# Performance work log

Hardware: AMD Instinct MI355X
Metric: run time of the kernel (lower is better)

Reference implementation:

```python
import jax, jax.numpy as jnp
import numpy as np

B, S, D = 2, 2048, 1024
H, DK = 16, 64          # heads, d_k (= d_v)
DH = 4096               # FFN hidden
EPS = 1e-5


def _layer_norm(x, gamma, beta):
    mu = jnp.mean(x, axis=-1, keepdims=True)
    var = jnp.var(x, axis=-1, keepdims=True)
    return (x - mu) * jax.lax.rsqrt(var + EPS) * gamma + beta


def setup_inputs() -> dict:
    key = jax.random.key(0)
    ks = jax.random.split(key, 8)
    s = lambda fan_in: 1.0 / np.sqrt(fan_in)
    return {
        "x": jax.random.normal(ks[0], (B, S, D), dtype=jnp.float32),
        # NOTE: source module uses W_q for queries, keys AND values (bug kept faithfully),
        # so W_k / W_v are never used and are not materialized.
        "Wq": jax.random.normal(ks[1], (D, H * DK), dtype=jnp.float32) * s(D),
        "bq": jnp.zeros((H * DK,), dtype=jnp.float32),
        "Wo": jax.random.normal(ks[2], (H * DK, D), dtype=jnp.float32) * s(H * DK),
        "bo": jnp.zeros((D,), dtype=jnp.float32),
        "ln1_g": jnp.ones((D,), dtype=jnp.float32),
        "ln1_b": jnp.zeros((D,), dtype=jnp.float32),
        "W1": jax.random.normal(ks[3], (D, DH), dtype=jnp.float32) * s(D),
        "b1": jnp.zeros((DH,), dtype=jnp.float32),
        "W2": jax.random.normal(ks[4], (DH, D), dtype=jnp.float32) * s(DH),
        "b2": jnp.zeros((D,), dtype=jnp.float32),
        "ln2_g": jnp.ones((D,), dtype=jnp.float32),
        "ln2_b": jnp.zeros((D,), dtype=jnp.float32),
    }


def reference(x, Wq, bq, Wo, bo, ln1_g, ln1_b, W1, b1, W2, b2, ln2_g, ln2_b):
    residual = x
    # projections: q, k, v all use W_q (faithful to source)
    q = (x @ Wq + bq).reshape(B, S, H, DK)
    k = (x @ Wq + bq).reshape(B, S, H, DK)
    v = (x @ Wq + bq).reshape(B, S, H, DK)
    # scores scaled by sqrt(sequence_length), as in the source
    scale = 1.0 / jnp.sqrt(jnp.float32(S))
    scores = jnp.einsum("bqhd,bkhd->bhqk", q, k) * scale
    probs = jax.nn.softmax(scores, axis=-1)
    attn = jnp.einsum("bhqk,bkhd->bqhd", probs, v).reshape(B, S, H * DK)
    attn = attn @ Wo + bo
    # dropout is identity in eval mode
    x = _layer_norm(attn + residual, ln1_g, ln1_b)
    residual = x
    h = jax.nn.relu(x @ W1 + b1)
    x = h @ W2 + b2
    x = _layer_norm(x + residual, ln2_g, ln2_b)
    return x
```

## Files before the change

### kernel.cpp

```cpp
#include <hip/hip_runtime.h>
#include <stdint.h>


typedef unsigned short u16;
typedef __attribute__((ext_vector_type(8))) short v8s;
typedef __attribute__((ext_vector_type(4))) float v4f;
typedef __attribute__((ext_vector_type(16))) float v16f;
typedef __attribute__((ext_vector_type(2))) unsigned int v2u;

#define AS1 __attribute__((address_space(1)))
#define AS3 __attribute__((address_space(3)))

__device__ __forceinline__ void gl_lds16(const u16* g, u16* l) {
  __builtin_amdgcn_global_load_lds((const AS1 void*)g, (AS3 void*)l, 16, 0, 0);
}

__device__ __forceinline__ float bf2f(u16 u) {
  union { uint32_t i; float f; } v; v.i = ((uint32_t)u) << 16; return v.f;
}
__device__ __forceinline__ u16 f2bf(float f) {
  union { float f; uint32_t i; } v; v.f = f;
  uint32_t x = v.i;
  return (u16)((x + 0x7FFFu + ((x >> 16) & 1u)) >> 16);
}
__device__ __forceinline__ uint32_t fbits(float f) {
  union { float f; uint32_t u; } v; v.f = f; return v.u;
}

__global__ __launch_bounds__(256) void cvt_f2b(
    const float* __restrict__ src, u16* __restrict__ dst, int n4) {
  int i = (blockIdx.x * 256 + threadIdx.x);
  if (i < n4) {
    float4 v = *(const float4*)(src + (size_t)i * 4);
    ushort4 o;
    o.x = f2bf(v.x); o.y = f2bf(v.y); o.z = f2bf(v.z); o.w = f2bf(v.w);
    *(ushort4*)(dst + (size_t)i * 4) = o;
  }
}

__global__ __launch_bounds__(256) void transpose_f2b(
    const float* __restrict__ src, u16* __restrict__ dst,
    int R, int C, int ld_s, int ld_d) {
  __shared__ float tile[32][33];
  const int tx = threadIdx.x & 31, ty = threadIdx.x >> 5;
  const int c0 = blockIdx.x * 32, r0 = blockIdx.y * 32;
#pragma unroll
  for (int j = 0; j < 32; j += 8)
    tile[ty + j][tx] = src[(size_t)(r0 + ty + j) * ld_s + c0 + tx];
  __syncthreads();
#pragma unroll
  for (int j = 0; j < 32; j += 8)
    dst[(size_t)(c0 + ty + j) * ld_d + r0 + tx] = f2bf(tile[tx][ty + j]);
}

__global__ __launch_bounds__(256) void transpose_b2b(
    const u16* __restrict__ src, u16* __restrict__ dst,
    int R, int C, int ld_s, int ld_d) {
  __shared__ u16 tile[32][33];
  const int tx = threadIdx.x & 31, ty = threadIdx.x >> 5;
  const int c0 = blockIdx.x * 32, r0 = blockIdx.y * 32;
#pragma unroll
  for (int j = 0; j < 32; j += 8)
    tile[ty + j][tx] = src[(size_t)(r0 + ty + j) * ld_s + c0 + tx];
  __syncthreads();
#pragma unroll
  for (int j = 0; j < 32; j += 8)
    dst[(size_t)(c0 + ty + j) * ld_d + r0 + tx] = tile[tx][ty + j];
}

__global__ __launch_bounds__(512, 1) void gemm_8p(
    const u16* __restrict__ A, const u16* __restrict__ Bt,
    const float* __restrict__ bias, void* __restrict__ C0,
    u16* __restrict__ C1, u16* __restrict__ C2, u16* __restrict__ C3,
    int M, int N, int ldk, int klen, int relu, int c0_f32) {
  __shared__ u16 As[2][16384];
  __shared__ u16 Bs[2][16384];
  const int tid = threadIdx.x;
  const int w = tid >> 6, l = tid & 63;
  const int l16 = l & 15, kgrp = (l >> 4) & 3;
  const int wm = w >> 2, wn = w & 3;

  const int gx = gridDim.x, gyd = gridDim.y;
  const int nxy = gx * gyd;
  const int nwg = nxy * gridDim.z;
  int lin = blockIdx.x + gx * (blockIdx.y + gyd * blockIdx.z);
  if ((nwg & 7) == 0) lin = (lin & 7) * (nwg >> 3) + (lin >> 3);
  const int z = lin / nxy;
  const int rem = lin - z * nxy;
  const int by = rem / gx;
  const int bx = rem - by * gx;
  const int m0 = by * 256, n0 = bx * 256;
  const int NT = klen >> 6;

  const int rl = tid >> 3;
  const int sw = 8 * ((tid & 7) ^ (rl & 7));
  const u16* gA[4]; const u16* gB[4];
#pragma unroll
  for (int j = 0; j < 4; j++) {
    gA[j] = A + (size_t)(m0 + j * 64 + rl) * ldk + (size_t)z * klen + sw;
    gB[j] = Bt + (size_t)(n0 + j * 64 + rl) * ldk + (size_t)z * klen + sw;
  }
  const int sdst = w * 512;

  const int ch0 = 8 * ((kgrp) ^ (l16 & 7));
  const int ch1 = 8 * ((4 + kgrp) ^ (l16 & 7));
  const int abase = (wm * 128 + l16) * 64;
  const int bbase = (wn * 64 + l16) * 64;

  v4f acc[8][4];
#pragma unroll
  for (int i = 0; i < 8; i++)
#pragma unroll
    for (int j = 0; j < 4; j++)
#pragma unroll
      for (int r = 0; r < 4; r++) acc[i][j][r] = 0.f;

  v8s a[4][2], b[4][2];

#define FENCE() asm volatile("" ::: "memory")
#define VMC(n) asm volatile("s_waitcnt vmcnt(" #n ")" ::: "memory")
#define BARX() { __builtin_amdgcn_s_barrier(); \
                 __builtin_amdgcn_sched_barrier(0); FENCE(); }
#define STGA(q, j, kt) gl_lds16(gA[j] + (size_t)(kt) * 64, &As[q][(j) * 4096 + sdst])
#define STGB(q, j, kt) gl_lds16(gB[j] + (size_t)(kt) * 64, &Bs[q][(j) * 4096 + sdst])
#define LDA(p, mh) { \
  const u16* Ap = &As[p][abase + (mh) * 4096]; \
  _Pragma("unroll") for (int mi = 0; mi < 4; mi++) { \
    a[mi][0] = *(const v8s*)(Ap + mi * 1024 + ch0); \
    a[mi][1] = *(const v8s*)(Ap + mi * 1024 + ch1); } }
#define LDB(p, nh) { \
  const u16* Bp = &Bs[p][bbase + (nh) * 2048]; \
  _Pragma("unroll") for (int ni = 0; ni < 2; ni++) { \
    b[(nh) * 2 + ni][0] = *(const v8s*)(Bp + ni * 1024 + ch0); \
    b[(nh) * 2 + ni][1] = *(const v8s*)(Bp + ni * 1024 + ch1); } }
#define MFQ(mh, nh) { \
  __builtin_amdgcn_s_setprio(1); \
  _Pragma("unroll") for (int ks = 0; ks < 2; ks++) \
  _Pragma("unroll") for (int mi = 0; mi < 4; mi++) \
  _Pragma("unroll") for (int ni = 0; ni < 2; ni++) \
    acc[(mh) * 4 + mi][(nh) * 2 + ni] = __builtin_amdgcn_mfma_f32_16x16x32_bf16( \
        a[mi][ks], b[(nh) * 2 + ni][ks], acc[(mh) * 4 + mi][(nh) * 2 + ni], 0, 0, 0); \
  __builtin_amdgcn_s_setprio(0); }

  STGA(0, 0, 0); STGA(0, 2, 0);
  FENCE();
  STGB(0, 0, 0); STGB(0, 1, 0);
  FENCE();
  STGB(0, 2, 0); STGB(0, 3, 0);
  FENCE();
  STGA(0, 1, 0); STGA(0, 3, 0);

  int p = 0;
  for (int kt = 0; kt < NT - 1; ++kt, p ^= 1) {
    const int q = p ^ 1;
    const int kn = kt + 1;
    VMC(2); BARX();
    LDA(p, 0);
    LDB(p, 0);
    FENCE();
    STGA(q, 0, kn); STGA(q, 2, kn);
    MFQ(0, 0);
    LDB(p, 1);
    FENCE();
    STGB(q, 0, kn); STGB(q, 1, kn);
    STGB(q, 2, kn); STGB(q, 3, kn);
    MFQ(0, 1);
    VMC(6); BARX();
    LDA(p, 1);
    FENCE();
    STGA(q, 1, kn); STGA(q, 3, kn);
    MFQ(1, 1);
    MFQ(1, 0);
  }
  VMC(0); BARX();
  LDA(p, 0);
  LDB(p, 0);
  MFQ(0, 0);
  LDB(p, 1);
  MFQ(0, 1);
  LDA(p, 1);
  MFQ(1, 1);
  MFQ(1, 0);

#undef FENCE
#undef VMC
#undef BARX
#undef STGA
#undef STGB
#undef LDA
#undef LDB
#undef MFQ

#pragma unroll
  for (int mi = 0; mi < 8; mi++) {
    const int row = m0 + wm * 128 + mi * 16 + kgrp * 4;
#pragma unroll
    for (int ni = 0; ni < 4; ni++) {
      const int col = n0 + wn * 64 + ni * 16 + l16;
      float bv = (bias && z == 0) ? bias[col] : 0.f;
#pragma unroll
      for (int r = 0; r < 4; r++) {
        float v = acc[mi][ni][r] + bv;
        if (z == 0 && relu) v = fmaxf(v, 0.f);
        size_t idx = (size_t)(row + r) * N + col;
        if (z == 0) {
          if (c0_f32) ((float*)C0)[idx] = v;
          else ((u16*)C0)[idx] = f2bf(v);
        } else if (z == 1) {
          C1[idx] = f2bf(v);
        } else if (z == 2) {
          C2[idx] = f2bf(v);
        } else {
          C3[idx] = f2bf(v);
        }
      }
    }
  }
}

__global__ __launch_bounds__(256) void gemm_g2(
    const u16* __restrict__ A, const u16* __restrict__ Bt,
    const float* __restrict__ bias, void* __restrict__ C,
    int M, int N, int K, int relu, int accum, int out_f32) {
  __shared__ u16 As[2][8192];
  __shared__ u16 Bs[2][4096];
  const int tid = threadIdx.x;
  const int w = tid >> 6, l = tid & 63;
  const int l16 = l & 15, kgrp = l >> 4;
  const int m0 = blockIdx.y * 128, n0 = blockIdx.x * 64;
  const int wr = (w >> 1) * 64, wc = (w & 1) * 32;

  const int srow = w * 8 + (l >> 3);
  const u16* gA[4];
#pragma unroll
  for (int i = 0; i < 4; i++) {
    int r = i * 32 + srow;
    gA[i] = A + (size_t)(m0 + r) * K + 8 * ((l & 7) ^ (r & 7));
  }
  const u16* gB[2];
#pragma unroll
  for (int i = 0; i < 2; i++) {
    int r = i * 32 + srow;
    gB[i] = Bt + (size_t)(n0 + r) * K + 8 * ((l & 7) ^ (r & 7));
  }

  v4f acc[4][2];
#pragma unroll
  for (int i = 0; i < 4; i++)
#pragma unroll
    for (int j = 0; j < 2; j++)
#pragma unroll
      for (int r = 0; r < 4; r++) acc[i][j][r] = 0.f;

#pragma unroll
  for (int i = 0; i < 4; i++) gl_lds16(gA[i], &As[0][(i * 256 + w * 64) * 8]);
#pragma unroll
  for (int i = 0; i < 2; i++) gl_lds16(gB[i], &Bs[0][(i * 256 + w * 64) * 8]);

  int cur = 0;
  for (int k0 = 0; k0 < K; k0 += 64) {
    __syncthreads();
    if (k0 + 64 < K) {
      int nxt = cur ^ 1;
#pragma unroll
      for (int i = 0; i < 4; i++)
        gl_lds16(gA[i] + k0 + 64, &As[nxt][(i * 256 + w * 64) * 8]);
#pragma unroll
      for (int i = 0; i < 2; i++)
        gl_lds16(gB[i] + k0 + 64, &Bs[nxt][(i * 256 + w * 64) * 8]);
    }
    v8s a[4][2], b[2][2];
#pragma unroll
    for (int ks = 0; ks < 2; ks++) {
      int ch = 8 * ((ks * 4 + kgrp) ^ (l16 & 7));
#pragma unroll
      for (int mi = 0; mi < 4; mi++)
        a[mi][ks] = *(const v8s*)(&As[cur][(wr + mi * 16 + l16) * 64 + ch]);
#pragma unroll
      for (int ni = 0; ni < 2; ni++)
        b[ni][ks] = *(const v8s*)(&Bs[cur][(wc + ni * 16 + l16) * 64 + ch]);
    }
#pragma unroll
    for (int ks = 0; ks < 2; ks++)
#pragma unroll
      for (int mi = 0; mi < 4; mi++)
#pragma unroll
        for (int ni = 0; ni < 2; ni++)
          acc[mi][ni] = __builtin_amdgcn_mfma_f32_16x16x32_bf16(a[mi][ks], b[ni][ks], acc[mi][ni], 0, 0, 0);
    cur ^= 1;
  }

#pragma unroll
  for (int ni = 0; ni < 2; ni++) {
    int col = n0 + wc + ni * 16 + l16;
    float bv = bias ? bias[col] : 0.f;
#pragma unroll
    for (int mi = 0; mi < 4; mi++) {
      int row = m0 + wr + mi * 16 + kgrp * 4;
#pragma unroll
      for (int r = 0; r < 4; r++) {
        float v = acc[mi][ni][r] + bv;
        if (relu) v = fmaxf(v, 0.f);
        size_t idx = (size_t)(row + r) * N + col;
        if (out_f32) {
          float* Cf = (float*)C;
          if (accum) v += Cf[idx];
          Cf[idx] = v;
        } else {
          ((u16*)C)[idx] = f2bf(v);
        }
      }
    }
  }
}

__global__ __launch_bounds__(512) void attn_kernel(
    const u16* __restrict__ Q, const u16* __restrict__ Qt,
    u16* __restrict__ O) {
  __shared__ u16 KV[2][8192];
  const int tid = threadIdx.x;
  const int w = tid >> 6, l = tid & 63;
  const int l31 = l & 31, hi = l >> 5;
  const int bh = blockIdx.y, b = bh >> 4, h = bh & 15;
  const int q0 = blockIdx.x * 256;
  const size_t rowQ = (size_t)(b * 2048 + q0 + w * 32);
  const float cexp = 1.4426950408889634f / 45.254833995939045f;

  const int isV = w >> 2, wl = w & 3;
  const int r0 = wl * 16 + (l >> 3);
  const int sch8 = 8 * ((l & 7) ^ (l >> 3));
  const u16* gS0;
  size_t kstep;
  if (!isV) {
    gS0 = Q + (size_t)(b * 2048 + r0) * 1024 + h * 64 + sch8;
    kstep = 1024;
  } else {
    gS0 = Qt + (size_t)(h * 64 + r0) * 4096 + b * 2048 + sch8;
    kstep = 1;
  }
  const u16* gS1 = gS0 + (size_t)8 * (isV ? 4096 : 1024);
  const int ldst = isV * 4096 + wl * 1024;

  v8s qb[4];
#pragma unroll
  for (int t = 0; t < 4; t++) {
    v8s v = *(const v8s*)(Q + (rowQ + l31) * 1024 + h * 64 + t * 16 + hi * 8);
#pragma unroll
    for (int j = 0; j < 8; j++) v[j] = (short)f2bf(bf2f((u16)v[j]) * cexp);
    qb[t] = v;
  }

  v16f o0, o1;
#pragma unroll
  for (int r = 0; r < 16; r++) { o0[r] = 0.f; o1[r] = 0.f; }
  float ls = 0.f;

  gl_lds16(gS0, &KV[0][ldst]);
  gl_lds16(gS1, &KV[0][ldst + 512]);

  int cur = 0;
  for (int kb = 0; kb < 2048; kb += 64) {
    __syncthreads();
    if (kb + 64 < 2048) {
      int nxt = cur ^ 1;
      gl_lds16(gS0 + (size_t)(kb + 64) * kstep, &KV[nxt][ldst]);
      gl_lds16(gS1 + (size_t)(kb + 64) * kstep, &KV[nxt][ldst + 512]);
    }
    const u16* Ks = &KV[cur][0];
    const u16* Vt = &KV[cur][4096];

    v16f s0, s1;
#pragma unroll
    for (int r = 0; r < 16; r++) { s0[r] = 0.f; s1[r] = 0.f; }
#pragma unroll
    for (int t = 0; t < 4; t++) {
      const int c = 8 * ((2 * t + hi) ^ (l & 7));
      v8s ka0 = *(const v8s*)(Ks + l31 * 64 + c);
      v8s ka1 = *(const v8s*)(Ks + (32 + l31) * 64 + c);
      s0 = __builtin_amdgcn_mfma_f32_32x32x16_bf16(ka0, qb[t], s0, 0, 0, 0);
      s1 = __builtin_amdgcn_mfma_f32_32x32x16_bf16(ka1, qb[t], s1, 0, 0, 0);
    }

    float p0[16], p1[16];
#pragma unroll
    for (int r = 0; r < 16; r++) {
      p0[r] = __builtin_amdgcn_exp2f(s0[r]);
      p1[r] = __builtin_amdgcn_exp2f(s1[r]);
      ls += p0[r] + p1[r];
    }

#define PVSTEP(t, P) { \
      const int off = 8 * ((t) & 1); \
      uint32_t dw00 = __builtin_amdgcn_perm(fbits(P[off + 1]), fbits(P[off + 0]), 0x07060302u); \
      uint32_t dw01 = __builtin_amdgcn_perm(fbits(P[off + 3]), fbits(P[off + 2]), 0x07060302u); \
      uint32_t dw10 = __builtin_amdgcn_perm(fbits(P[off + 5]), fbits(P[off + 4]), 0x07060302u); \
      uint32_t dw11 = __builtin_amdgcn_perm(fbits(P[off + 7]), fbits(P[off + 6]), 0x07060302u); \
      v2u sA = __builtin_amdgcn_permlane32_swap(dw00, dw10, false, false); \
      v2u sB = __builtin_amdgcn_permlane32_swap(dw01, dw11, false, false); \
      union { uint32_t u[4]; v8s v; } pa; \
      pa.u[0] = sA[0]; pa.u[1] = sB[0]; pa.u[2] = sA[1]; pa.u[3] = sB[1]; \
      const int c = 8 * ((2 * (t) + hi) ^ (l & 7)); \
      v8s vb0 = *(const v8s*)(Vt + l31 * 64 + c); \
      v8s vb1 = *(const v8s*)(Vt + (32 + l31) * 64 + c); \
      o0 = __builtin_amdgcn_mfma_f32_32x32x16_bf16(pa.v, vb0, o0, 0, 0, 0); \
      o1 = __builtin_amdgcn_mfma_f32_32x32x16_bf16(pa.v, vb1, o1, 0, 0, 0); }
    PVSTEP(0, p0)
    PVSTEP(1, p0)
    PVSTEP(2, p1)
    PVSTEP(3, p1)
#undef PVSTEP
    cur ^= 1;
  }

  ls += __shfl_xor(ls, 32, 64);

  const int hiq = hi * 4;
#pragma unroll
  for (int r = 0; r < 16; r++) {
    const int qo = (r & 3) + 8 * (r >> 2) + hiq;
    float den = __shfl(ls, qo, 64);
    float rden = 1.f / den;
    O[(rowQ + qo) * 1024 + h * 64 + l31] = f2bf(o0[r] * rden);
    O[(rowQ + qo) * 1024 + h * 64 + 32 + l31] = f2bf(o1[r] * rden);
  }
}

__global__ __launch_bounds__(256) void ln_residual(
    const void* __restrict__ Y, const void* __restrict__ Y2,
    const void* __restrict__ Y3, const void* __restrict__ Y4,
    const void* __restrict__ Xr,
    const float* __restrict__ g, const float* __restrict__ bb,
    void* __restrict__ out, int yf, int y2f, int xf, int of) {
  const int row = blockIdx.x, tid = threadIdx.x;
  const size_t base = (size_t)row * 1024;
  float v[4], s = 0.f, sq = 0.f;
#pragma unroll
  for (int i = 0; i < 4; i++) {
    int c = tid + i * 256;
    float ya = yf ? ((const float*)Y)[base + c] : bf2f(((const u16*)Y)[base + c]);
    float xa = xf ? ((const float*)Xr)[base + c] : bf2f(((const u16*)Xr)[base + c]);
    float x = ya + xa;
    if (Y2) {
      float y2a = y2f ? ((const float*)Y2)[base + c] : bf2f(((const u16*)Y2)[base + c]);
      x += y2a;
    }
    if (Y3) x += bf2f(((const u16*)Y3)[base + c]);
    if (Y4) x += bf2f(((const u16*)Y4)[base + c]);
    v[i] = x; s += x; sq += x * x;
  }
#pragma unroll
  for (int off = 32; off >= 1; off >>= 1) {
    s += __shfl_down(s, off, 64);
    sq += __shfl_down(sq, off, 64);
  }
  __shared__ float rs[4], rq[4];
  const int w = tid >> 6, l = tid & 63;
  if (l == 0) { rs[w] = s; rq[w] = sq; }
  __syncthreads();
  s = rs[0] + rs[1] + rs[2] + rs[3];
  sq = rq[0] + rq[1] + rq[2] + rq[3];
  const float mu = s * (1.f / 1024.f);
  const float var = sq * (1.f / 1024.f) - mu * mu;
  const float rstd = rsqrtf(var + 1e-5f);
#pragma unroll
  for (int i = 0; i < 4; i++) {
    int c = tid + i * 256;
    float r = (v[i] - mu) * rstd * g[c] + bb[c];
    if (of) ((float*)out)[base + c] = r;
    else ((u16*)out)[base + c] = f2bf(r);
  }
}

extern "C" void kernel_launch(void* const* d_in, const int* in_sizes, int n_in,
                              void* d_out, int out_size, void* d_ws, size_t ws_size,
                              hipStream_t stream) {
  const float* x   = (const float*)d_in[0];
  const float* Wq  = (const float*)d_in[1];
  const float* bq  = (const float*)d_in[2];
  const float* Wo  = (const float*)d_in[3];
  const float* bo  = (const float*)d_in[4];
  const float* g1  = (const float*)d_in[5];
  const float* be1 = (const float*)d_in[6];
  const float* W1  = (const float*)d_in[7];
  const float* b1  = (const float*)d_in[8];
  const float* W2  = (const float*)d_in[9];
  const float* b2  = (const float*)d_in[10];
  const float* g2  = (const float*)d_in[11];
  const float* be2 = (const float*)d_in[12];
  float* out = (float*)d_out;
  u16* ws  = (u16*)d_ws;

  const size_t M1 = 1048576;
  dim3 blk(256);
  dim3 blk8(512);
  const bool big = ws_size >= (size_t)37 * M1 * 2;

  if (big) {
    u16* xb   = ws + 0;
    u16* Qb   = ws + 4 * M1;
    u16* Qt   = ws + 8 * M1;
    u16* WqT  = ws + 12 * M1;
    u16* W1T  = ws + 13 * M1;
    u16* W2T  = ws + 17 * M1;
    u16* Hh   = ws + 21 * M1;
    u16* attn = xb;  u16* Yb = Qt;  u16* x1 = Qb;  u16* WoT = WqT;
    u16* P1wo = W1T;
    u16* P2wo = W2T;
    u16* P3wo = Hh;
    u16* P1f2 = Qt;
    u16* P2f2 = xb;
    u16* P3f2 = W1T;

    cvt_f2b<<<dim3(4096), blk, 0, stream>>>(x, xb, 1048576);
    transpose_f2b<<<dim3(32, 32), blk, 0, stream>>>(Wq, WqT, 1024, 1024, 1024, 1024);
    gemm_g2<<<dim3(16, 32), blk, 0, stream>>>(xb, WqT, bq, Qb, 4096, 1024, 1024, 0, 0, 0);

    transpose_b2b<<<dim3(32, 128), blk, 0, stream>>>(Qb, Qt, 4096, 1024, 1024, 4096);
    attn_kernel<<<dim3(8, 32), blk8, 0, stream>>>(Qb, Qt, attn);

    transpose_f2b<<<dim3(32, 32), blk, 0, stream>>>(Wo, WoT, 1024, 1024, 1024, 1024);
    gemm_8p<<<dim3(4, 16, 4), blk8, 0, stream>>>(attn, WoT, bo, Yb, P1wo, P2wo, P3wo,
                                                 4096, 1024, 1024, 256, 0, 0);
    ln_residual<<<dim3(4096), blk, 0, stream>>>(Yb, P1wo, P2wo, P3wo, x, g1, be1, x1,
                                                0, 0, 1, 0);

    transpose_f2b<<<dim3(128, 32), blk, 0, stream>>>(W1, W1T, 1024, 4096, 4096, 1024);
    gemm_8p<<<dim3(16, 16, 1), blk8, 0, stream>>>(x1, W1T, b1, Hh,
                                                  nullptr, nullptr, nullptr,
                                                  4096, 4096, 1024, 1024, 1, 0);

    transpose_f2b<<<dim3(32, 128), blk, 0, stream>>>(W2, W2T, 4096, 1024, 1024, 4096);
    gemm_8p<<<dim3(4, 16, 4), blk8, 0, stream>>>(Hh, W2T, b2, out, P1f2, P2f2, P3f2,
                                                 4096, 1024, 4096, 1024, 0, 1);

    ln_residual<<<dim3(4096), blk, 0, stream>>>(out, P1f2, P2f2, P3f2, x1, g2, be2, out,
                                                1, 0, 0, 1);
  } else {
    u16* xb   = ws + 0;
    u16* Qb   = ws + 4 * M1;
    u16* Qt   = ws + 8 * M1;
    u16* attn = xb;  u16* Yb = Qt;  u16* x1 = Qb;  u16* Hc = xb;
    u16* Wt1  = ws + 12 * M1;
    u16* Wt2  = ws + 13 * M1;

    cvt_f2b<<<dim3(4096), blk, 0, stream>>>(x, xb, 1048576);
    transpose_f2b<<<dim3(32, 32), blk, 0, stream>>>(Wq, Wt1, 1024, 1024, 1024, 1024);
    gemm_g2<<<dim3(16, 32), blk, 0, stream>>>(xb, Wt1, bq, Qb, 4096, 1024, 1024, 0, 0, 0);

    transpose_b2b<<<dim3(32, 128), blk, 0, stream>>>(Qb, Qt, 4096, 1024, 1024, 4096);
    attn_kernel<<<dim3(8, 32), blk8, 0, stream>>>(Qb, Qt, attn);

    transpose_f2b<<<dim3(32, 32), blk, 0, stream>>>(Wo, Wt2, 1024, 1024, 1024, 1024);
    gemm_g2<<<dim3(16, 32), blk, 0, stream>>>(attn, Wt2, bo, Yb, 4096, 1024, 1024, 0, 0, 0);
    ln_residual<<<dim3(4096), blk, 0, stream>>>(Yb, nullptr, nullptr, nullptr, x, g1, be1,
                                                x1, 0, 0, 1, 0);

    for (int c = 0; c < 4; c++) {
      transpose_f2b<<<dim3(32, 32), blk, 0, stream>>>(W1 + (size_t)c * 1024, Wt1,
                                                      1024, 1024, 4096, 1024);
      gemm_g2<<<dim3(16, 32), blk, 0, stream>>>(x1, Wt1, b1 + (size_t)c * 1024, Hc,
                                                4096, 1024, 1024, 1, 0, 0);
      transpose_f2b<<<dim3(32, 32), blk, 0, stream>>>(W2 + (size_t)c * M1, Wt2,
                                                      1024, 1024, 1024, 1024);
      gemm_g2<<<dim3(16, 32), blk, 0, stream>>>(Hc, Wt2, (c == 0) ? b2 : (const float*)nullptr,
                                                out, 4096, 1024, 1024, 0, (c > 0) ? 1 : 0, 1);
    }
    ln_residual<<<dim3(4096), blk, 0, stream>>>(out, nullptr, nullptr, nullptr, x1, g2, be2,
                                                out, 1, 0, 0, 1);
  }
}
```

Before: 329.8 us.

## Process 64 query rows per wave in attention to reuse K/V fragments

The attention kernel now uses 4 waves of 256 threads instead of 8, and each wave owns 64 query rows (two 32-row tiles). Each K and V fragment read from LDS therefore feeds twice as many MFMAs, which cuts LDS read traffic per FLOP. Every wave now loads both K and V tiles, where before half the waves loaded K and half loaded V. s_setprio is also placed around the MFMA bursts. The cost is roughly double the accumulator and probability registers per wave and fewer waves per block, which could lower occupancy and latency hiding.

```diff
diff --git a/kernel.cpp b/kernel.cpp
--- a/kernel.cpp
+++ b/kernel.cpp
@@ -314,7 +314,7 @@
   }
 }
 
-__global__ __launch_bounds__(512) void attn_kernel(
+__global__ __launch_bounds__(256) void attn_kernel(
     const u16* __restrict__ Q, const u16* __restrict__ Qt,
     u16* __restrict__ O) {
   __shared__ u16 KV[2][8192];
@@ -323,105 +323,125 @@
   const int l31 = l & 31, hi = l >> 5;
   const int bh = blockIdx.y, b = bh >> 4, h = bh & 15;
   const int q0 = blockIdx.x * 256;
-  const size_t rowQ = (size_t)(b * 2048 + q0 + w * 32);
+  const size_t rowQ = (size_t)(b * 2048 + q0 + w * 64);
   const float cexp = 1.4426950408889634f / 45.254833995939045f;
 
-  const int isV = w >> 2, wl = w & 3;
-  const int r0 = wl * 16 + (l >> 3);
+  const int r0 = w * 16 + (l >> 3);
   const int sch8 = 8 * ((l & 7) ^ (l >> 3));
-  const u16* gS0;
-  size_t kstep;
-  if (!isV) {
-    gS0 = Q + (size_t)(b * 2048 + r0) * 1024 + h * 64 + sch8;
-    kstep = 1024;
-  } else {
-    gS0 = Qt + (size_t)(h * 64 + r0) * 4096 + b * 2048 + sch8;
-    kstep = 1;
-  }
-  const u16* gS1 = gS0 + (size_t)8 * (isV ? 4096 : 1024);
-  const int ldst = isV * 4096 + wl * 1024;
-
-  v8s qb[4];
+  const u16* gK = Q + (size_t)(b * 2048 + r0) * 1024 + h * 64 + sch8;
+  const u16* gK1 = gK + (size_t)8 * 1024;
+  const u16* gV = Qt + (size_t)(h * 64 + r0) * 4096 + b * 2048 + sch8;
+  const u16* gV1 = gV + (size_t)8 * 4096;
+  const int ldstK = w * 1024;
+  const int ldstV = 4096 + w * 1024;
+
+  v8s qa[4], qc[4];
 #pragma unroll
   for (int t = 0; t < 4; t++) {
-    v8s v = *(const v8s*)(Q + (rowQ + l31) * 1024 + h * 64 + t * 16 + hi * 8);
-#pragma unroll
-    for (int j = 0; j < 8; j++) v[j] = (short)f2bf(bf2f((u16)v[j]) * cexp);
-    qb[t] = v;
-  }
-
-  v16f o0, o1;
-#pragma unroll
-  for (int r = 0; r < 16; r++) { o0[r] = 0.f; o1[r] = 0.f; }
-  float ls = 0.f;
-
-  gl_lds16(gS0, &KV[0][ldst]);
-  gl_lds16(gS1, &KV[0][ldst + 512]);
+    v8s va = *(const v8s*)(Q + (rowQ + l31) * 1024 + h * 64 + t * 16 + hi * 8);
+    v8s vc = *(const v8s*)(Q + (rowQ + 32 + l31) * 1024 + h * 64 + t * 16 + hi * 8);
+#pragma unroll
+    for (int j = 0; j < 8; j++) {
+      va[j] = (short)f2bf(bf2f((u16)va[j]) * cexp);
+      vc[j] = (short)f2bf(bf2f((u16)vc[j]) * cexp);
+    }
+    qa[t] = va; qc[t] = vc;
+  }
+
+  v16f oA0, oA1, oB0, oB1;
+#pragma unroll
+  for (int r = 0; r < 16; r++) { oA0[r] = 0.f; oA1[r] = 0.f; oB0[r] = 0.f; oB1[r] = 0.f; }
+  float lsA = 0.f, lsB = 0.f;
+
+  gl_lds16(gK, &KV[0][ldstK]);
+  gl_lds16(gK1, &KV[0][ldstK + 512]);
+  gl_lds16(gV, &KV[0][ldstV]);
+  gl_lds16(gV1, &KV[0][ldstV + 512]);
 
   int cur = 0;
   for (int kb = 0; kb < 2048; kb += 64) {
     __syncthreads();
     if (kb + 64 < 2048) {
       int nxt = cur ^ 1;
-      gl_lds16(gS0 + (size_t)(kb + 64) * kstep, &KV[nxt][ldst]);
-      gl_lds16(gS1 + (size_t)(kb + 64) * kstep, &KV[nxt][ldst + 512]);
+      gl_lds16(gK + (size_t)(kb + 64) * 1024, &KV[nxt][ldstK]);
+      gl_lds16(gK1 + (size_t)(kb + 64) * 1024, &KV[nxt][ldstK + 512]);
+      gl_lds16(gV + (kb + 64), &KV[nxt][ldstV]);
+      gl_lds16(gV1 + (kb + 64), &KV[nxt][ldstV + 512]);
     }
     const u16* Ks = &KV[cur][0];
     const u16* Vt = &KV[cur][4096];
 
-    v16f s0, s1;
-#pragma unroll
-    for (int r = 0; r < 16; r++) { s0[r] = 0.f; s1[r] = 0.f; }
+    v16f s00, s10, s01, s11;
+#pragma unroll
+    for (int r = 0; r < 16; r++) { s00[r] = 0.f; s10[r] = 0.f; s01[r] = 0.f; s11[r] = 0.f; }
+    __builtin_amdgcn_s_setprio(1);
 #pragma unroll
     for (int t = 0; t < 4; t++) {
       const int c = 8 * ((2 * t + hi) ^ (l & 7));
       v8s ka0 = *(const v8s*)(Ks + l31 * 64 + c);
       v8s ka1 = *(const v8s*)(Ks + (32 + l31) * 64 + c);
-      s0 = __builtin_amdgcn_mfma_f32_32x32x16_bf16(ka0, qb[t], s0, 0, 0, 0);
-      s1 = __builtin_amdgcn_mfma_f32_32x32x16_bf16(ka1, qb[t], s1, 0, 0, 0);
-    }
-
-    float p0[16], p1[16];
+      s00 = __builtin_amdgcn_mfma_f32_32x32x16_bf16(ka0, qa[t], s00, 0, 0, 0);
+      s10 = __builtin_amdgcn_mfma_f32_32x32x16_bf16(ka1, qa[t], s10, 0, 0, 0);
+      s01 = __builtin_amdgcn_mfma_f32_32x32x16_bf16(ka0, qc[t], s01, 0, 0, 0);
+      s11 = __builtin_amdgcn_mfma_f32_32x32x16_bf16(ka1, qc[t], s11, 0, 0, 0);
+    }
+    __builtin_amdgcn_s_setprio(0);
+
+    float pA0[16], pA1[16], pB0[16], pB1[16];
 #pragma unroll
     for (int r = 0; r < 16; r++) {
-      p0[r] = __builtin_amdgcn_exp2f(s0[r]);
-      p1[r] = __builtin_amdgcn_exp2f(s1[r]);
-      ls += p0[r] + p1[r];
-    }
-
-#define PVSTEP(t, P) { \
-      const int off = 8 * ((t) & 1); \
+      pA0[r] = __builtin_amdgcn_exp2f(s00[r]);
+      pA1[r] = __builtin_amdgcn_exp2f(s10[r]);
+      pB0[r] = __builtin_amdgcn_exp2f(s01[r]);
+      pB1[r] = __builtin_amdgcn_exp2f(s11[r]);
+      lsA += pA0[r] + pA1[r];
+      lsB += pB0[r] + pB1[r];
+    }
+
+#define PACKP(P, out) { \
+      const int off = 8 * ((tt) & 1); \
       uint32_t dw00 = __builtin_amdgcn_perm(fbits(P[off + 1]), fbits(P[off + 0]), 0x07060302u); \
       uint32_t dw01 = __builtin_amdgcn_perm(fbits(P[off + 3]), fbits(P[off + 2]), 0x07060302u); \
       uint32_t dw10 = __builtin_amdgcn_perm(fbits(P[off + 5]), fbits(P[off + 4]), 0x07060302u); \
       uint32_t dw11 = __builtin_amdgcn_perm(fbits(P[off + 7]), fbits(P[off + 6]), 0x07060302u); \
-      v2u sA = __builtin_amdgcn_permlane32_swap(dw00, dw10, false, false); \
-      v2u sB = __builtin_amdgcn_permlane32_swap(dw01, dw11, false, false); \
-      union { uint32_t u[4]; v8s v; } pa; \
-      pa.u[0] = sA[0]; pa.u[1] = sB[0]; pa.u[2] = sA[1]; pa.u[3] = sB[1]; \
-      const int c = 8 * ((2 * (t) + hi) ^ (l & 7)); \
+      v2u sA_ = __builtin_amdgcn_permlane32_swap(dw00, dw10, false, false); \
+      v2u sB_ = __builtin_amdgcn_permlane32_swap(dw01, dw11, false, false); \
+      out.u[0] = sA_[0]; out.u[1] = sB_[0]; out.u[2] = sA_[1]; out.u[3] = sB_[1]; }
+#define PVSTEP(t, PA, PB) { \
+      const int tt = (t); \
+      union { uint32_t u[4]; v8s v; } paA, paB; \
+      PACKP(PA, paA); \
+      PACKP(PB, paB); \
+      const int c = 8 * ((2 * tt + hi) ^ (l & 7)); \
       v8s vb0 = *(const v8s*)(Vt + l31 * 64 + c); \
       v8s vb1 = *(const v8s*)(Vt + (32 + l31) * 64 + c); \
-      o0 = __builtin_amdgcn_mfma_f32_32x32x16_bf16(pa.v, vb0, o0, 0, 0, 0); \
-      o1 = __builtin_amdgcn_mfma_f32_32x32x16_bf16(pa.v, vb1, o1, 0, 0, 0); }
-    PVSTEP(0, p0)
-    PVSTEP(1, p0)
-    PVSTEP(2, p1)
-    PVSTEP(3, p1)
+      __builtin_amdgcn_s_setprio(1); \
+      oA0 = __builtin_amdgcn_mfma_f32_32x32x16_bf16(paA.v, vb0, oA0, 0, 0, 0); \
+      oA1 = __builtin_amdgcn_mfma_f32_32x32x16_bf16(paA.v, vb1, oA1, 0, 0, 0); \
+      oB0 = __builtin_amdgcn_mfma_f32_32x32x16_bf16(paB.v, vb0, oB0, 0, 0, 0); \
+      oB1 = __builtin_amdgcn_mfma_f32_32x32x16_bf16(paB.v, vb1, oB1, 0, 0, 0); \
+      __builtin_amdgcn_s_setprio(0); }
+    PVSTEP(0, pA0, pB0)
+    PVSTEP(1, pA0, pB0)
+    PVSTEP(2, pA1, pB1)
+    PVSTEP(3, pA1, pB1)
 #undef PVSTEP
+#undef PACKP
     cur ^= 1;
   }
 
-  ls += __shfl_xor(ls, 32, 64);
-
-  const int hiq = hi * 4;
+  lsA += __shfl_xor(lsA, 32, 64);
+  lsB += __shfl_xor(lsB, 32, 64);
+
 #pragma unroll
   for (int r = 0; r < 16; r++) {
-    const int qo = (r & 3) + 8 * (r >> 2) + hiq;
-    float den = __shfl(ls, qo, 64);
-    float rden = 1.f / den;
-    O[(rowQ + qo) * 1024 + h * 64 + l31] = f2bf(o0[r] * rden);
-    O[(rowQ + qo) * 1024 + h * 64 + 32 + l31] = f2bf(o1[r] * rden);
+    const int qo = (r & 3) + 8 * (r >> 2) + hi * 4;
+    float rdA = 1.f / __shfl(lsA, qo, 64);
+    float rdB = 1.f / __shfl(lsB, qo, 64);
+    O[(rowQ + qo) * 1024 + h * 64 + l31] = f2bf(oA0[r] * rdA);
+    O[(rowQ + qo) * 1024 + h * 64 + 32 + l31] = f2bf(oA1[r] * rdA);
+    O[(rowQ + 32 + qo) * 1024 + h * 64 + l31] = f2bf(oB0[r] * rdB);
+    O[(rowQ + 32 + qo) * 1024 + h * 64 + 32 + l31] = f2bf(oB1[r] * rdB);
   }
 }
 
@@ -516,7 +536,7 @@
     gemm_g2<<<dim3(16, 32), blk, 0, stream>>>(xb, WqT, bq, Qb, 4096, 1024, 1024, 0, 0, 0);
 
     transpose_b2b<<<dim3(32, 128), blk, 0, stream>>>(Qb, Qt, 4096, 1024, 1024, 4096);
-    attn_kernel<<<dim3(8, 32), blk8, 0, stream>>>(Qb, Qt, attn);
+    attn_kernel<<<dim3(8, 32), blk, 0, stream>>>(Qb, Qt, attn);
 
     transpose_f2b<<<dim3(32, 32), blk, 0, stream>>>(Wo, WoT, 1024, 1024, 1024, 1024);
     gemm_8p<<<dim3(4, 16, 4), blk8, 0, stream>>>(attn, WoT, bo, Yb, P1wo, P2wo, P3wo,
@@ -548,7 +568,7 @@
     gemm_g2<<<dim3(16, 32), blk, 0, stream>>>(xb, Wt1, bq, Qb, 4096, 1024, 1024, 0, 0, 0);
 
     transpose_b2b<<<dim3(32, 128), blk, 0, stream>>>(Qb, Qt, 4096, 1024, 1024, 4096);
-    attn_kernel<<<dim3(8, 32), blk8, 0, stream>>>(Qb, Qt, attn);
+    attn_kernel<<<dim3(8, 32), blk, 0, stream>>>(Qb, Qt, attn);
 
     transpose_f2b<<<dim3(32, 32), blk, 0, stream>>>(Wo, Wt2, 1024, 1024, 1024, 1024);
     gemm_g2<<<dim3(16, 32), blk, 0, stream>>>(attn, Wt2, bo, Yb, 4096, 1024, 1024, 0, 0, 0);
```

Result: slower. 341.8 us (+3.6%).

## Split attention over KV halves with larger per-wave query tiles and combine pass

Applied to the files above, without the earlier changes.

Replaces the single attention kernel with a split-KV version in which each block covers 512 queries and half of the key/value range. Each wave now handles 64 queries, so every K/V tile loaded into LDS feeds twice as many MFMAs. Partial outputs and row sums are written in fp32 and merged by a separate combine kernel. This adds fp32 partial traffic (about 32MB written and read back) and one extra launch. It also relies on unnormalized exp2 with no running max, which is safe only because the scores stay small.

```diff
diff --git a/kernel.cpp b/kernel.cpp
--- a/kernel.cpp
+++ b/kernel.cpp
@@ -314,6 +314,159 @@
   }
 }
 
+__global__ __launch_bounds__(512) void attn_split(
+    const u16* __restrict__ Q, const u16* __restrict__ Qt,
+    float* __restrict__ Op, float* __restrict__ lsp) {
+  __shared__ u16 KV[2][8192];
+  const int tid = threadIdx.x;
+  const int w = tid >> 6, l = tid & 63;
+  const int l31 = l & 31, hi = l >> 5;
+  const int bh = blockIdx.y, b = bh >> 4, h = bh & 15;
+  const int q0 = blockIdx.x * 512;
+  const int z = blockIdx.z;
+  const int kv0 = z * 1024;
+  const size_t rowQ = (size_t)(b * 2048 + q0 + w * 64);
+  const float cexp = 1.4426950408889634f / 45.254833995939045f;
+
+  const int isV = w >> 2, wl = w & 3;
+  const int r0 = wl * 16 + (l >> 3);
+  const int sch8 = 8 * ((l & 7) ^ (l >> 3));
+  const u16* gS0;
+  size_t kstep;
+  if (!isV) {
+    gS0 = Q + (size_t)(b * 2048 + kv0 + r0) * 1024 + h * 64 + sch8;
+    kstep = 1024;
+  } else {
+    gS0 = Qt + (size_t)(h * 64 + r0) * 4096 + b * 2048 + kv0 + sch8;
+    kstep = 1;
+  }
+  const u16* gS1 = gS0 + (size_t)8 * (isV ? 4096 : 1024);
+  const int ldst = isV * 4096 + wl * 1024;
+
+  v8s qa[4], qc[4];
+#pragma unroll
+  for (int t = 0; t < 4; t++) {
+    v8s va = *(const v8s*)(Q + (rowQ + l31) * 1024 + h * 64 + t * 16 + hi * 8);
+    v8s vc = *(const v8s*)(Q + (rowQ + 32 + l31) * 1024 + h * 64 + t * 16 + hi * 8);
+#pragma unroll
+    for (int j = 0; j < 8; j++) {
+      va[j] = (short)f2bf(bf2f((u16)va[j]) * cexp);
+      vc[j] = (short)f2bf(bf2f((u16)vc[j]) * cexp);
+    }
+    qa[t] = va; qc[t] = vc;
+  }
+
+  v16f oA0, oA1, oB0, oB1;
+#pragma unroll
+  for (int r = 0; r < 16; r++) { oA0[r] = 0.f; oA1[r] = 0.f; oB0[r] = 0.f; oB1[r] = 0.f; }
+  float lsA = 0.f, lsB = 0.f;
+
+  gl_lds16(gS0, &KV[0][ldst]);
+  gl_lds16(gS1, &KV[0][ldst + 512]);
+
+  int cur = 0;
+  for (int kb = 0; kb < 1024; kb += 64) {
+    __syncthreads();
+    if (kb + 64 < 1024) {
+      int nxt = cur ^ 1;
+      gl_lds16(gS0 + (size_t)(kb + 64) * kstep, &KV[nxt][ldst]);
+      gl_lds16(gS1 + (size_t)(kb + 64) * kstep, &KV[nxt][ldst + 512]);
+    }
+    const u16* Ks = &KV[cur][0];
+    const u16* Vt = &KV[cur][4096];
+
+    v16f s00, s10, s01, s11;
+#pragma unroll
+    for (int r = 0; r < 16; r++) { s00[r] = 0.f; s10[r] = 0.f; s01[r] = 0.f; s11[r] = 0.f; }
+    __builtin_amdgcn_s_setprio(1);
+#pragma unroll
+    for (int t = 0; t < 4; t++) {
+      const int c = 8 * ((2 * t + hi) ^ (l & 7));
+      v8s ka0 = *(const v8s*)(Ks + l31 * 64 + c);
+      v8s ka1 = *(const v8s*)(Ks + (32 + l31) * 64 + c);
+      s00 = __builtin_amdgcn_mfma_f32_32x32x16_bf16(ka0, qa[t], s00, 0, 0, 0);
+      s10 = __builtin_amdgcn_mfma_f32_32x32x16_bf16(ka1, qa[t], s10, 0, 0, 0);
+      s01 = __builtin_amdgcn_mfma_f32_32x32x16_bf16(ka0, qc[t], s01, 0, 0, 0);
+      s11 = __builtin_amdgcn_mfma_f32_32x32x16_bf16(ka1, qc[t], s11, 0, 0, 0);
+    }
+    __builtin_amdgcn_s_setprio(0);
+
+    float pA0[16], pA1[16], pB0[16], pB1[16];
+#pragma unroll
+    for (int r = 0; r < 16; r++) {
+      pA0[r] = __builtin_amdgcn_exp2f(s00[r]);
+      pA1[r] = __builtin_amdgcn_exp2f(s10[r]);
+      pB0[r] = __builtin_amdgcn_exp2f(s01[r]);
+      pB1[r] = __builtin_amdgcn_exp2f(s11[r]);
+      lsA += pA0[r] + pA1[r];
+      lsB += pB0[r] + pB1[r];
+    }
+
+#define PACKP(P, out) { \
+      const int off = 8 * ((tt) & 1); \
+      uint32_t dw00 = __builtin_amdgcn_perm(fbits(P[off + 1]), fbits(P[off + 0]), 0x07060302u); \
+      uint32_t dw01 = __builtin_amdgcn_perm(fbits(P[off + 3]), fbits(P[off + 2]), 0x07060302u); \
+      uint32_t dw10 = __builtin_amdgcn_perm(fbits(P[off + 5]), fbits(P[off + 4]), 0x07060302u); \
+      uint32_t dw11 = __builtin_amdgcn_perm(fbits(P[off + 7]), fbits(P[off + 6]), 0x07060302u); \
+      v2u sA_ = __builtin_amdgcn_permlane32_swap(dw00, dw10, false, false); \
+      v2u sB_ = __builtin_amdgcn_permlane32_swap(dw01, dw11, false, false); \
+      out.u[0] = sA_[0]; out.u[1] = sB_[0]; out.u[2] = sA_[1]; out.u[3] = sB_[1]; }
+#define PVSTEP(t, PA, PB) { \
+      const int tt = (t); \
+      union { uint32_t u[4]; v8s v; } paA, paB; \
+      PACKP(PA, paA); \
+      PACKP(PB, paB); \
+      const int c = 8 * ((2 * tt + hi) ^ (l & 7)); \
+      v8s vb0 = *(const v8s*)(Vt + l31 * 64 + c); \
+      v8s vb1 = *(const v8s*)(Vt + (32 + l31) * 64 + c); \
+      __builtin_amdgcn_s_setprio(1); \
+      oA0 = __builtin_amdgcn_mfma_f32_32x32x16_bf16(paA.v, vb0, oA0, 0, 0, 0); \
+      oA1 = __builtin_amdgcn_mfma_f32_32x32x16_bf16(paA.v, vb1, oA1, 0, 0, 0); \
+      oB0 = __builtin_amdgcn_mfma_f32_32x32x16_bf16(paB.v, vb0, oB0, 0, 0, 0); \
+      oB1 = __builtin_amdgcn_mfma_f32_32x32x16_bf16(paB.v, vb1, oB1, 0, 0, 0); \
+      __builtin_amdgcn_s_setprio(0); }
+    PVSTEP(0, pA0, pB0)
+    PVSTEP(1, pA0, pB0)
+    PVSTEP(2, pA1, pB1)
+    PVSTEP(3, pA1, pB1)
+#undef PVSTEP
+#undef PACKP
+    cur ^= 1;
+  }
+
+  lsA += __shfl_xor(lsA, 32, 64);
+  lsB += __shfl_xor(lsB, 32, 64);
+
+  float* OPz = Op + (size_t)z * 4194304;
+#pragma unroll
+  for (int r = 0; r < 16; r++) {
+    const int qo = (r & 3) + 8 * (r >> 2) + hi * 4;
+    OPz[(rowQ + qo) * 1024 + h * 64 + l31] = oA0[r];
+    OPz[(rowQ + qo) * 1024 + h * 64 + 32 + l31] = oA1[r];
+    OPz[(rowQ + 32 + qo) * 1024 + h * 64 + l31] = oB0[r];
+    OPz[(rowQ + 32 + qo) * 1024 + h * 64 + 32 + l31] = oB1[r];
+  }
+  if (hi == 0) {
+    lsp[(size_t)z * 65536 + (rowQ + l31) * 16 + h] = lsA;
+    lsp[(size_t)z * 65536 + (rowQ + 32 + l31) * 16 + h] = lsB;
+  }
+}
+
+__global__ __launch_bounds__(256) void attn_combine(
+    const float* __restrict__ Op, const float* __restrict__ lsp,
+    u16* __restrict__ O) {
+  const int row = blockIdx.x, tid = threadIdx.x;
+  const size_t base = (size_t)row * 1024;
+#pragma unroll
+  for (int i = 0; i < 4; i++) {
+    int c = tid + i * 256;
+    int h = c >> 6;
+    float den = lsp[(size_t)row * 16 + h] + lsp[65536 + (size_t)row * 16 + h];
+    float o = Op[base + c] + Op[4194304 + base + c];
+    O[base + c] = f2bf(o / den);
+  }
+}
+
 __global__ __launch_bounds__(512) void attn_kernel(
     const u16* __restrict__ Q, const u16* __restrict__ Qt,
     u16* __restrict__ O) {
@@ -504,6 +657,8 @@
     u16* W2T  = ws + 17 * M1;
     u16* Hh   = ws + 21 * M1;
     u16* attn = xb;  u16* Yb = Qt;  u16* x1 = Qb;  u16* WoT = WqT;
+    float* Opart = (float*)(ws + 13 * M1);
+    float* lspart = (float*)(ws + 29 * M1);
     u16* P1wo = W1T;
     u16* P2wo = W2T;
     u16* P3wo = Hh;
@@ -516,7 +671,8 @@
     gemm_g2<<<dim3(16, 32), blk, 0, stream>>>(xb, WqT, bq, Qb, 4096, 1024, 1024, 0, 0, 0);
 
     transpose_b2b<<<dim3(32, 128), blk, 0, stream>>>(Qb, Qt, 4096, 1024, 1024, 4096);
-    attn_kernel<<<dim3(8, 32), blk8, 0, stream>>>(Qb, Qt, attn);
+    attn_split<<<dim3(4, 32, 2), blk8, 0, stream>>>(Qb, Qt, Opart, lspart);
+    attn_combine<<<dim3(4096), blk, 0, stream>>>(Opart, lspart, attn);
 
     transpose_f2b<<<dim3(32, 32), blk, 0, stream>>>(Wo, WoT, 1024, 1024, 1024, 1024);
     gemm_8p<<<dim3(4, 16, 4), blk8, 0, stream>>>(attn, WoT, bo, Yb, P1wo, P2wo, P3wo,
```

Result: slower. 341.7 us (+3.6%).

## Fuse all weight transposes and input conversion into one prep launch; remap attention blocks

Applied to the files above, without the earlier changes.

Merges the x fp32-to-bf16 conversion and the four weight transpose-conversions into a single prep_all kernel launched once up front. The workspace layout is rearranged so WoT and the Wo-GEMM partial buffers get their own regions and are not overwritten. The aim is fewer kernel launches and less serialisation between small kernels. The attention kernel also remaps its linear block index in a stride-8 pattern, likely to spread neighbouring workgroups across XCDs. In exchange the workspace footprint grows and all transpose work is front-loaded before the first GEMM.

```diff
diff --git a/kernel.cpp b/kernel.cpp
--- a/kernel.cpp
+++ b/kernel.cpp
@@ -36,6 +36,39 @@
     o.x = f2bf(v.x); o.y = f2bf(v.y); o.z = f2bf(v.z); o.w = f2bf(v.w);
     *(ushort4*)(dst + (size_t)i * 4) = o;
   }
+}
+
+__global__ __launch_bounds__(256) void prep_all(
+    const float* __restrict__ x, const float* __restrict__ Wq,
+    const float* __restrict__ Wo, const float* __restrict__ W1,
+    const float* __restrict__ W2, u16* __restrict__ xb,
+    u16* __restrict__ WqT, u16* __restrict__ WoT,
+    u16* __restrict__ W1T, u16* __restrict__ W2T) {
+  const int r = blockIdx.x;
+  const int tid = threadIdx.x;
+  if (r >= 10240) {
+    int i = (r - 10240) * 256 + tid;
+    float4 v = *(const float4*)(x + (size_t)i * 4);
+    ushort4 o;
+    o.x = f2bf(v.x); o.y = f2bf(v.y); o.z = f2bf(v.z); o.w = f2bf(v.w);
+    *(ushort4*)(xb + (size_t)i * 4) = o;
+    return;
+  }
+  __shared__ float tile[32][33];
+  const float* src; u16* dst; int ld_s, ld_d, bx, by;
+  if (r < 1024)      { src = Wq; dst = WqT; ld_s = 1024; ld_d = 1024; bx = r & 31; by = r >> 5; }
+  else if (r < 2048) { int r2 = r - 1024; src = Wo; dst = WoT; ld_s = 1024; ld_d = 1024; bx = r2 & 31; by = r2 >> 5; }
+  else if (r < 6144) { int r2 = r - 2048; src = W1; dst = W1T; ld_s = 4096; ld_d = 1024; bx = r2 & 127; by = r2 >> 7; }
+  else               { int r2 = r - 6144; src = W2; dst = W2T; ld_s = 1024; ld_d = 4096; bx = r2 & 31; by = r2 >> 5; }
+  const int tx = tid & 31, ty = tid >> 5;
+  const int c0 = bx * 32, r0 = by * 32;
+#pragma unroll
+  for (int j = 0; j < 32; j += 8)
+    tile[ty + j][tx] = src[(size_t)(r0 + ty + j) * ld_s + c0 + tx];
+  __syncthreads();
+#pragma unroll
+  for (int j = 0; j < 32; j += 8)
+    dst[(size_t)(c0 + ty + j) * ld_d + r0 + tx] = f2bf(tile[tx][ty + j]);
 }
 
 __global__ __launch_bounds__(256) void transpose_f2b(
@@ -321,8 +354,15 @@
   const int tid = threadIdx.x;
   const int w = tid >> 6, l = tid & 63;
   const int l31 = l & 31, hi = l >> 5;
-  const int bh = blockIdx.y, b = bh >> 4, h = bh & 15;
-  const int q0 = blockIdx.x * 256;
+
+  const int gx = gridDim.x;
+  const int nwg = gx * gridDim.y;
+  int lin = blockIdx.x + gx * blockIdx.y;
+  if ((nwg & 7) == 0) lin = (lin & 7) * (nwg >> 3) + (lin >> 3);
+  const int bxi = lin % gx;
+  const int bh = lin / gx;
+  const int b = bh >> 4, h = bh & 15;
+  const int q0 = bxi * 256;
   const size_t rowQ = (size_t)(b * 2048 + q0 + w * 32);
   const float cexp = 1.4426950408889634f / 45.254833995939045f;
 
@@ -503,36 +543,29 @@
     u16* W1T  = ws + 13 * M1;
     u16* W2T  = ws + 17 * M1;
     u16* Hh   = ws + 21 * M1;
-    u16* attn = xb;  u16* Yb = Qt;  u16* x1 = Qb;  u16* WoT = WqT;
-    u16* P1wo = W1T;
-    u16* P2wo = W2T;
-    u16* P3wo = Hh;
+    u16* P1wo = ws + 21 * M1;
+    u16* P2wo = ws + 25 * M1;
+    u16* P3wo = ws + 29 * M1;
+    u16* WoT  = ws + 33 * M1;
+    u16* attn = xb;  u16* Yb = Qt;  u16* x1 = Qb;
     u16* P1f2 = Qt;
     u16* P2f2 = xb;
     u16* P3f2 = W1T;
 
-    cvt_f2b<<<dim3(4096), blk, 0, stream>>>(x, xb, 1048576);
-    transpose_f2b<<<dim3(32, 32), blk, 0, stream>>>(Wq, WqT, 1024, 1024, 1024, 1024);
+    prep_all<<<dim3(14336), blk, 0, stream>>>(x, Wq, Wo, W1, W2,
+                                              xb, WqT, WoT, W1T, W2T);
     gemm_g2<<<dim3(16, 32), blk, 0, stream>>>(xb, WqT, bq, Qb, 4096, 1024, 1024, 0, 0, 0);
-
     transpose_b2b<<<dim3(32, 128), blk, 0, stream>>>(Qb, Qt, 4096, 1024, 1024, 4096);
     attn_kernel<<<dim3(8, 32), blk8, 0, stream>>>(Qb, Qt, attn);
-
-    transpose_f2b<<<dim3(32, 32), blk, 0, stream>>>(Wo, WoT, 1024, 1024, 1024, 1024);
     gemm_8p<<<dim3(4, 16, 4), blk8, 0, stream>>>(attn, WoT, bo, Yb, P1wo, P2wo, P3wo,
                                                  4096, 1024, 1024, 256, 0, 0);
     ln_residual<<<dim3(4096), blk, 0, stream>>>(Yb, P1wo, P2wo, P3wo, x, g1, be1, x1,
                                                 0, 0, 1, 0);
-
-    transpose_f2b<<<dim3(128, 32), blk, 0, stream>>>(W1, W1T, 1024, 4096, 4096, 1024);
     gemm_8p<<<dim3(16, 16, 1), blk8, 0, stream>>>(x1, W1T, b1, Hh,
                                                   nullptr, nullptr, nullptr,
                                                   4096, 4096, 1024, 1024, 1, 0);
-
-    transpose_f2b<<<dim3(32, 128), blk, 0, stream>>>(W2, W2T, 4096, 1024, 1024, 4096);
     gemm_8p<<<dim3(4, 16, 4), blk8, 0, stream>>>(Hh, W2T, b2, out, P1f2, P2f2, P3f2,
                                                  4096, 1024, 4096, 1024, 0, 1);
-
     ln_residual<<<dim3(4096), blk, 0, stream>>>(out, P1f2, P2f2, P3f2, x1, g2, be2, out,
                                                 1, 0, 0, 1);
   } else {
```

After: 321.9 us. 1.02x faster.
